# Kernel optimization log

Measured on AMD Instinct MI355X. Metric: run time of the kernel, lower is better.

The kernel has to match this reference:

```python
import jax, jax.numpy as jnp
import numpy as np

N, M, D, L = 8, 2048, 128, 128  # batch, num_nodes, input_dim, latent_dim


def setup_inputs() -> dict:
    key = jax.random.key(0)
    ks = jax.random.split(key, 9)
    s = 0.02
    return {
        "x": jax.random.normal(ks[0], (N, M, D), dtype=jnp.float32),
        # f_node: Linear(D, 2L) -> ReLU -> Linear(2L, L)
        "w1n": jax.random.normal(ks[1], (D, 2 * L), dtype=jnp.float32) * s,
        "b1n": jnp.zeros((2 * L,), dtype=jnp.float32),
        "w2n": jax.random.normal(ks[2], (2 * L, L), dtype=jnp.float32) * s,
        "b2n": jnp.zeros((L,), dtype=jnp.float32),
        # f_edge: Linear(2L, L) -> ReLU -> Linear(L, 1)
        "w1e": jax.random.normal(ks[3], (2 * L, L), dtype=jnp.float32) * s,
        "b1e": jnp.zeros((L,), dtype=jnp.float32),
        "w2e": jax.random.normal(ks[4], (L, 1), dtype=jnp.float32) * s,
        "b2e": jnp.zeros((1,), dtype=jnp.float32),
    }


def reference(x, w1n, b1n, w2n, b2n, w1e, b1e, w2e, b2e):
    n, m, _ = x.shape
    # f_node MLP: (N, m, D) -> (N, m, L)
    h = jnp.maximum(x @ w1n + b1n, 0.0) @ w2n + b2n
    # In the original, the double transpose on `receiver` cancels, so the
    # edge feature is concat(x_i, x_i) for every (i, j) pair: independent of j.
    # Compute per-node then broadcast across j (identical math, no O(m^2 * 2L) blowup).
    pair = jnp.concatenate([h, h], axis=-1)              # (N, m, 2L)
    e = jnp.maximum(pair @ w1e + b1e, 0.0) @ w2e + b2e   # (N, m, 1)
    e = e / m
    edge = jnp.broadcast_to(e, (n, m, m))                # edge[b, i, j] = e[b, i]
    return h, edge
```

## Files before the change

kernel.cpp:

```cpp
#include <hip/hip_runtime.h>


typedef short short8 __attribute__((ext_vector_type(8)));
typedef float floatx4 __attribute__((ext_vector_type(4)));

__device__ __forceinline__ short f2bf(float f) {
    union { float f; unsigned u; } v; v.f = f;
    unsigned r = v.u + 0x7fffu + ((v.u >> 16) & 1u);
    return (short)(r >> 16);
}

__global__ __launch_bounds__(256)
void prep_weights(const float* __restrict__ w1n, const float* __restrict__ w2n,
                  const float* __restrict__ w1e, short* __restrict__ ws)
{
    const int id = blockIdx.x * 256 + threadIdx.x;
    if (id < 32768) {
        const int n = id >> 7, k = id & 127;
        ws[id] = f2bf(w1n[k * 256 + n]);
    } else if (id < 65536) {
        const int j = id - 32768;
        const int n = j >> 8, k = j & 255;
        ws[id] = f2bf(w2n[k * 128 + n]);
    } else {
        const int j = id - 65536;
        const int n = j >> 7, k = j & 127;
        ws[id] = f2bf(w1e[k * 128 + n] + w1e[(k + 128) * 128 + n]);
    }
}

#define TPB 256
#define ROWS 16
#define XS_STRIDE 136
#define H1_STRIDE 264

__global__ __launch_bounds__(TPB, 4)
void fused_node_edge(const float* __restrict__ x,
                     const float* __restrict__ b1n, const float* __restrict__ b2n,
                     const float* __restrict__ b1e,
                     const float* __restrict__ w2e, const float* __restrict__ b2e,
                     const short* __restrict__ wt,
                     float* __restrict__ h_out, float* __restrict__ edge_out)
{
    __shared__ short xs[ROWS * XS_STRIDE];
    __shared__ short h1s[ROWS * H1_STRIDE];
    __shared__ short hbs[ROWS * XS_STRIDE];
    __shared__ float partial[4][ROWS];
    __shared__ float es[ROWS];

    const int t = threadIdx.x;
    const int w = t >> 6;
    const int l = t & 63;
    const int l15 = l & 15;
    const int quad = l >> 4;
    const int row0 = blockIdx.x * ROWS;

    {
        const float4* __restrict__ x4 = (const float4*)(x + (size_t)row0 * 128);
#pragma unroll
        for (int i = 0; i < 2; ++i) {
            const int fi = t + i * TPB;
            const float4 v = x4[fi];
            const int row = fi >> 5, col = (fi & 31) * 4;
            short4 s;
            s.x = f2bf(v.x); s.y = f2bf(v.y); s.z = f2bf(v.z); s.w = f2bf(v.w);
            *(short4*)&xs[row * XS_STRIDE + col] = s;
        }
    }
    __syncthreads();

    {
        short8 a1[4];
#pragma unroll
        for (int k = 0; k < 4; ++k)
            a1[k] = *(const short8*)&xs[l15 * XS_STRIDE + k * 32 + quad * 8];

        floatx4 acc1[4];
#pragma unroll
        for (int ci = 0; ci < 4; ++ci) {
            const int ct = 4 * w + ci;
            const float b = b1n[ct * 16 + l15];
            acc1[ci] = (floatx4){b, b, b, b};
#pragma unroll
            for (int k = 0; k < 4; ++k) {
                const short8 bf = *(const short8*)(wt + (ct * 16 + l15) * 128 + k * 32 + quad * 8);
                acc1[ci] = __builtin_amdgcn_mfma_f32_16x16x32_bf16(a1[k], bf, acc1[ci], 0, 0, 0);
            }
        }
#pragma unroll
        for (int ci = 0; ci < 4; ++ci) {
            const int ct = 4 * w + ci;
#pragma unroll
            for (int r = 0; r < 4; ++r)
                h1s[(quad * 4 + r) * H1_STRIDE + ct * 16 + l15] = f2bf(fmaxf(acc1[ci][r], 0.f));
        }
    }
    __syncthreads();

    {
        short8 a2[8];
#pragma unroll
        for (int k = 0; k < 8; ++k)
            a2[k] = *(const short8*)&h1s[l15 * H1_STRIDE + k * 32 + quad * 8];

        const short* __restrict__ W2T = wt + 32768;
#pragma unroll
        for (int ci = 0; ci < 2; ++ci) {
            const int ct = 2 * w + ci;
            const float b = b2n[ct * 16 + l15];
            floatx4 acc2 = (floatx4){b, b, b, b};
#pragma unroll
            for (int k = 0; k < 8; ++k) {
                const short8 bf = *(const short8*)(W2T + (ct * 16 + l15) * 256 + k * 32 + quad * 8);
                acc2 = __builtin_amdgcn_mfma_f32_16x16x32_bf16(a2[k], bf, acc2, 0, 0, 0);
            }
#pragma unroll
            for (int r = 0; r < 4; ++r) {
                const int row = quad * 4 + r;
                const float v = acc2[r];
                h_out[(size_t)(row0 + row) * 128 + ct * 16 + l15] = v;
                hbs[row * XS_STRIDE + ct * 16 + l15] = f2bf(v);
            }
        }
    }
    __syncthreads();

    {
        short8 a3[4];
#pragma unroll
        for (int k = 0; k < 4; ++k)
            a3[k] = *(const short8*)&hbs[l15 * XS_STRIDE + k * 32 + quad * 8];

        const short* __restrict__ WET = wt + 65536;
        float p[4] = {0.f, 0.f, 0.f, 0.f};
#pragma unroll
        for (int ci = 0; ci < 2; ++ci) {
            const int ct = 2 * w + ci;
            const float b = b1e[ct * 16 + l15];
            floatx4 acc3 = (floatx4){b, b, b, b};
#pragma unroll
            for (int k = 0; k < 4; ++k) {
                const short8 bf = *(const short8*)(WET + (ct * 16 + l15) * 128 + k * 32 + quad * 8);
                acc3 = __builtin_amdgcn_mfma_f32_16x16x32_bf16(a3[k], bf, acc3, 0, 0, 0);
            }
            const float wv = w2e[ct * 16 + l15];
#pragma unroll
            for (int r = 0; r < 4; ++r)
                p[r] += fmaxf(acc3[r], 0.f) * wv;
        }
#pragma unroll
        for (int off = 8; off >= 1; off >>= 1)
#pragma unroll
            for (int r = 0; r < 4; ++r)
                p[r] += __shfl_xor(p[r], off, 64);
        if (l15 == 0) {
#pragma unroll
            for (int r = 0; r < 4; ++r)
                partial[w][quad * 4 + r] = p[r];
        }
    }
    __syncthreads();
    if (t < ROWS) {
        es[t] = (partial[0][t] + partial[1][t] + partial[2][t] + partial[3][t]
                 + b2e[0]) * (1.0f / 2048.0f);
    }
    __syncthreads();

    {
        floatx4* __restrict__ e4 = (floatx4*)(edge_out + (size_t)row0 * 2048);
#pragma unroll 4
        for (int r = 0; r < ROWS; ++r) {
            const float ev = es[r];
            const floatx4 vv = (floatx4){ev, ev, ev, ev};
            __builtin_nontemporal_store(vv, &e4[r * 512 + t]);
            __builtin_nontemporal_store(vv, &e4[r * 512 + t + 256]);
        }
    }
}

extern "C" void kernel_launch(void* const* d_in, const int* in_sizes, int n_in,
                              void* d_out, int out_size, void* d_ws, size_t ws_size,
                              hipStream_t stream) {
    const float* x   = (const float*)d_in[0];
    const float* w1n = (const float*)d_in[1];
    const float* b1n = (const float*)d_in[2];
    const float* w2n = (const float*)d_in[3];
    const float* b2n = (const float*)d_in[4];
    const float* w1e = (const float*)d_in[5];
    const float* b1e = (const float*)d_in[6];
    const float* w2e = (const float*)d_in[7];
    const float* b2e = (const float*)d_in[8];

    float* h_out    = (float*)d_out;
    float* edge_out = (float*)d_out + (size_t)8 * 2048 * 128;
    short* wt       = (short*)d_ws;

    prep_weights<<<dim3(320), dim3(256), 0, stream>>>(w1n, w2n, w1e, wt);
    fused_node_edge<<<dim3(1024), dim3(TPB), 0, stream>>>(
        x, b1n, b2n, b1e, w2e, b2e, wt, h_out, edge_out);
}
```

Before: 182.4 us.

## Split edge broadcast into a separate kernel with regular stores

The per-row edge scalars are now written to a workspace buffer, and a new kernel broadcasts them into the 128 MB edge output. That kernel uses 4096 blocks of four waves, each wave filling one row with plain (not nontemporal) float4 stores. The aim is to decouple the write-bandwidth-bound broadcast from the MFMA compute kernel so the large store stream gets more parallelism and better occupancy. The cost is an extra kernel launch, a small workspace round trip, and the loss of nontemporal store hints.

After: 184.0 us. No clear change (+0.8%).

```diff
diff --git a/kernel.cpp b/kernel.cpp
--- a/kernel.cpp
+++ b/kernel.cpp
@@ -35,18 +35,17 @@
 #define H1_STRIDE 264
 
 __global__ __launch_bounds__(TPB, 4)
-void fused_node_edge(const float* __restrict__ x,
-                     const float* __restrict__ b1n, const float* __restrict__ b2n,
-                     const float* __restrict__ b1e,
-                     const float* __restrict__ w2e, const float* __restrict__ b2e,
-                     const short* __restrict__ wt,
-                     float* __restrict__ h_out, float* __restrict__ edge_out)
+void node_edge_compute(const float* __restrict__ x,
+                       const float* __restrict__ b1n, const float* __restrict__ b2n,
+                       const float* __restrict__ b1e,
+                       const float* __restrict__ w2e, const float* __restrict__ b2e,
+                       const short* __restrict__ wt,
+                       float* __restrict__ h_out, float* __restrict__ e_ws)
 {
     __shared__ short xs[ROWS * XS_STRIDE];
     __shared__ short h1s[ROWS * H1_STRIDE];
     __shared__ short hbs[ROWS * XS_STRIDE];
     __shared__ float partial[4][ROWS];
-    __shared__ float es[ROWS];
 
     const int t = threadIdx.x;
     const int w = t >> 6;
@@ -161,21 +160,23 @@
     }
     __syncthreads();
     if (t < ROWS) {
-        es[t] = (partial[0][t] + partial[1][t] + partial[2][t] + partial[3][t]
-                 + b2e[0]) * (1.0f / 2048.0f);
-    }
-    __syncthreads();
-
-    {
-        floatx4* __restrict__ e4 = (floatx4*)(edge_out + (size_t)row0 * 2048);
-#pragma unroll 4
-        for (int r = 0; r < ROWS; ++r) {
-            const float ev = es[r];
-            const floatx4 vv = (floatx4){ev, ev, ev, ev};
-            __builtin_nontemporal_store(vv, &e4[r * 512 + t]);
-            __builtin_nontemporal_store(vv, &e4[r * 512 + t + 256]);
-        }
-    }
+        e_ws[row0 + t] = (partial[0][t] + partial[1][t] + partial[2][t]
+                          + partial[3][t] + b2e[0]) * (1.0f / 2048.0f);
+    }
+}
+
+__global__ __launch_bounds__(256)
+void edge_broadcast(const float* __restrict__ es, float* __restrict__ edge_out)
+{
+    const int t = threadIdx.x;
+    const int row = blockIdx.x * 4 + (t >> 6);
+    const int l = t & 63;
+    const float ev = es[row];
+    floatx4* __restrict__ e4 = (floatx4*)(edge_out + (size_t)row * 2048);
+    const floatx4 vv = (floatx4){ev, ev, ev, ev};
+#pragma unroll
+    for (int i = 0; i < 8; ++i)
+        e4[i * 64 + l] = vv;
 }
 
 extern "C" void kernel_launch(void* const* d_in, const int* in_sizes, int n_in,
@@ -194,8 +195,10 @@
     float* h_out    = (float*)d_out;
     float* edge_out = (float*)d_out + (size_t)8 * 2048 * 128;
     short* wt       = (short*)d_ws;
+    float* e_ws     = (float*)((char*)d_ws + 163840);
 
     prep_weights<<<dim3(320), dim3(256), 0, stream>>>(w1n, w2n, w1e, wt);
-    fused_node_edge<<<dim3(1024), dim3(TPB), 0, stream>>>(
-        x, b1n, b2n, b1e, w2e, b2e, wt, h_out, edge_out);
-}
+    node_edge_compute<<<dim3(1024), dim3(TPB), 0, stream>>>(
+        x, b1n, b2n, b1e, w2e, b2e, wt, h_out, e_ws);
+    edge_broadcast<<<dim3(4096), dim3(256), 0, stream>>>(e_ws, edge_out);
+}
```
